# Performance work log

Measured on AMD Instinct MI355X. Metric: run time of the kernel, lower is better.

## Reference

```python
import jax, jax.numpy as jnp
import numpy as np

N = 131072   # total nodes
B = 256      # graphs
NPG = 512    # nodes per graph (N = B*NPG, nodes ordered by graph)
K = 7        # knn neighbors
H = 4        # heads


def setup_inputs() -> dict:
    key = jax.random.key(0)
    ks = jax.random.split(key, 16)
    s = 0.1
    pos = jax.random.normal(ks[0], (N, 3), jnp.float32)
    x = jax.random.normal(ks[1], (N, 10), jnp.float32)
    batch = jnp.repeat(jnp.arange(B, dtype=jnp.int32), NPG)
    # GATv2 layer 1: in=10, out=16, heads=4 -> H*C = 64
    Wl1 = jax.random.normal(ks[2], (10, 64), jnp.float32) * s
    bl1 = jnp.zeros((64,), jnp.float32)
    Wr1 = jax.random.normal(ks[3], (10, 64), jnp.float32) * s
    br1 = jnp.zeros((64,), jnp.float32)
    att1 = jax.random.normal(ks[4], (H, 16), jnp.float32) * s
    bias1 = jnp.zeros((64,), jnp.float32)
    # GATv2 layer 2: in=64, out=32, heads=4 -> H*C = 128
    Wl2 = jax.random.normal(ks[5], (64, 128), jnp.float32) * s
    bl2 = jnp.zeros((128,), jnp.float32)
    Wr2 = jax.random.normal(ks[6], (64, 128), jnp.float32) * s
    br2 = jnp.zeros((128,), jnp.float32)
    att2 = jax.random.normal(ks[7], (H, 32), jnp.float32) * s
    bias2 = jnp.zeros((128,), jnp.float32)
    return dict(pos=pos, x=x, batch=batch,
                Wl1=Wl1, bl1=bl1, Wr1=Wr1, br1=br1, att1=att1, bias1=bias1,
                Wl2=Wl2, bl2=bl2, Wr2=Wr2, br2=br2, att2=att2, bias2=bias2)


def knn_edges(pos):
    # equal-size graphs, nodes ordered by graph -> per-graph brute-force kNN
    p = pos.reshape(B, NPG, -1)                                  # [B,n,3]
    d2 = jnp.sum((p[:, :, None, :] - p[:, None, :, :]) ** 2, -1)  # [B,n,n]
    d2 = d2 + jnp.eye(NPG, dtype=d2.dtype) * 1e10                 # no self-loops
    _, idx = jax.lax.top_k(-d2, K)                                # [B,n,K]
    offs = (jnp.arange(B, dtype=idx.dtype) * NPG)[:, None, None]
    src = (idx + offs).reshape(-1)                                # neighbors -> sources
    dst = jnp.broadcast_to(jnp.arange(N)[:, None], (N, K)).reshape(-1)
    return src, dst


def gatv2(x, src, dst, Wl, bl, Wr, br, att, C):
    xl = (x @ Wl + bl).reshape(N, H, C)   # lin_l -> source features / messages
    xr = (x @ Wr + br).reshape(N, H, C)   # lin_r -> target features
    m = jax.nn.leaky_relu(xl[src] + xr[dst], 0.2)     # [E,H,C]
    alpha = jnp.einsum('ehc,hc->eh', m, att)          # [E,H]
    amax = jax.ops.segment_max(alpha, dst, num_segments=N)
    ea = jnp.exp(alpha - amax[dst])
    denom = jax.ops.segment_sum(ea, dst, num_segments=N)
    a = ea / denom[dst]                               # softmax per destination
    out = jax.ops.segment_sum(a[:, :, None] * xl[src], dst, num_segments=N)
    return out.reshape(N, H * C)


def reference(pos, x, batch, Wl1, bl1, Wr1, br1, att1, bias1,
              Wl2, bl2, Wr2, br2, att2, bias2):
    src, dst = knn_edges(pos)
    h = gatv2(x, src, dst, Wl1, bl1, Wr1, br1, att1, 16) + bias1   # [N,64]
    h = gatv2(h, src, dst, Wl2, bl2, Wr2, br2, att2, 32) + bias2   # [N,128]
    # global mean pool over batch ids
    sums = jax.ops.segment_sum(h, batch, num_segments=B)
    cnts = jax.ops.segment_sum(jnp.ones((N, 1), h.dtype), batch, num_segments=B)
    return sums / cnts                                              # [B,128]
```

## Files before the change

### kernel.cpp

```cpp
#include <hip/hip_runtime.h>
#include <hip/hip_bf16.h>

#define N_NODES 131072
#define B_GRAPHS 256
#define NPG 512
#define KNN 7
#define HEADS 4

using f4 = __attribute__((ext_vector_type(4))) float;
using short8 = __attribute__((ext_vector_type(8))) short;

__device__ __forceinline__ unsigned short f2bf(float f) {
    unsigned u = __builtin_bit_cast(unsigned, f);
    u += 0x7FFFu + ((u >> 16) & 1u);
    return (unsigned short)(u >> 16);
}

__device__ __forceinline__ void s8_to_f(const short8 v, f4* out) {
#pragma unroll
    for (int i = 0; i < 8; ++i) {
        const unsigned u = ((unsigned)(unsigned short)v[i]) << 16;
        out[i >> 2][i & 3] = __builtin_bit_cast(float, u);
    }
}

__device__ __forceinline__ unsigned med3u(unsigned a, unsigned b, unsigned c) {
    unsigned r;
    asm("v_med3_u32 %0, %1, %2, %3" : "=v"(r) : "v"(a), "v"(b), "v"(c));
    return r;
}

#define INS7(B, KEY) { \
    const unsigned _k = (KEY); \
    const unsigned n0 = min(B[0], _k); \
    const unsigned n1 = med3u(B[0], B[1], _k); \
    const unsigned n2 = med3u(B[1], B[2], _k); \
    const unsigned n3 = med3u(B[2], B[3], _k); \
    const unsigned n4 = med3u(B[3], B[4], _k); \
    const unsigned n5 = med3u(B[4], B[5], _k); \
    const unsigned n6 = med3u(B[5], B[6], _k); \
    B[0]=n0; B[1]=n1; B[2]=n2; B[3]=n3; B[4]=n4; B[5]=n5; B[6]=n6; }

__global__ __launch_bounds__(512) void knn_kernel(const float* __restrict__ pos,
                                                  int* __restrict__ knn) {
    __shared__ f4 sp[NPG];
    __shared__ unsigned mk[3][128][7];
    const int tid = threadIdx.x;
    const int g = blockIdx.x >> 2;
    const int qh = blockIdx.x & 3;
    const int ch = tid >> 7;
    const int ql = tid & 127;
    const int q = qh * 128 + ql;

    const float* p = pos + (size_t)g * NPG * 3;
    {
        f4 v; v[0] = p[tid * 3 + 0]; v[1] = p[tid * 3 + 1]; v[2] = p[tid * 3 + 2]; v[3] = 0.f;
        sp[tid] = v;
    }
    __syncthreads();

    const f4 qp = sp[q];
    unsigned b[7];
#pragma unroll
    for (int i = 0; i < 7; ++i) b[i] = 0xFFFFFFFFu;

    const int j0 = ch << 7;
#pragma unroll 8
    for (int j = 0; j < 128; ++j) {
        const int jj = j0 + j;
        const f4 c = sp[jj];
        const float dx = qp[0] - c[0];
        const float dy = qp[1] - c[1];
        const float dz = qp[2] - c[2];
        const float d2 = dx * dx + dy * dy + dz * dz;
        unsigned key = (__builtin_bit_cast(unsigned, d2) & 0xFFFFFE00u) | (unsigned)jj;
        key = (jj == q) ? 0xFFFFFFFFu : key;
        INS7(b, key)
    }

    if (ch != 0) {
        unsigned* m = mk[ch - 1][ql];
#pragma unroll
        for (int i = 0; i < 7; ++i) m[i] = b[i];
    }
    __syncthreads();
    if (ch == 0) {
#pragma unroll
        for (int cc = 0; cc < 3; ++cc) {
            const unsigned* m = mk[cc][ql];
#pragma unroll
            for (int i = 0; i < 7; ++i) INS7(b, m[i])
        }
        const int base = (g * NPG + q) * KNN;
        const int off = g * NPG;
#pragma unroll
        for (int i = 0; i < 7; ++i) knn[base + i] = off + (int)(b[i] & 0x1FFu);
    }
}
#undef INS7

__global__ __launch_bounds__(256) void lin1_kernel(const float* __restrict__ x,
                                                   const float* __restrict__ Wl,
                                                   const float* __restrict__ bl,
                                                   const float* __restrict__ Wr,
                                                   const float* __restrict__ br,
                                                   unsigned short* __restrict__ xl1b,
                                                   float* __restrict__ xr1) {
    const int idx = blockIdx.x * 256 + threadIdx.x;
    const int c4 = idx & 15;
    const size_t node = (size_t)(idx >> 4);
    const float* xrow = x + node * 10;
    f4 al = ((const f4*)bl)[c4];
    f4 ar = ((const f4*)br)[c4];
#pragma unroll
    for (int k = 0; k < 10; ++k) {
        const float xv = xrow[k];
        al += xv * ((const f4*)(Wl + k * 64))[c4];
        ar += xv * ((const f4*)(Wr + k * 64))[c4];
    }
    uint2 pk;
    pk.x = (unsigned)f2bf(al[0]) | ((unsigned)f2bf(al[1]) << 16);
    pk.y = (unsigned)f2bf(al[2]) | ((unsigned)f2bf(al[3]) << 16);
    ((uint2*)xl1b)[node * 16 + c4] = pk;
    ((f4*)(xr1 + node * 64))[c4] = ar;
}

__global__ __launch_bounds__(256) void agg1_kernel(const unsigned short* __restrict__ xl1b,
                                                   const float* __restrict__ xr,
                                                   const int* __restrict__ knn,
                                                   const float* __restrict__ att,
                                                   const float* __restrict__ bias,
                                                   unsigned short* __restrict__ h1b) {
    const int x = blockIdx.x & 7;
    const int i = blockIdx.x >> 3;
    const int graph = x * 32 + (i >> 3);
    const int sub = i & 7;
    const int tid = threadIdx.x;
    const int h = tid & 3;
    const size_t node = (size_t)graph * NPG + sub * 64 + (tid >> 2);

    const int* nb = knn + node * KNN;
    int j[KNN];
#pragma unroll
    for (int k = 0; k < KNN; ++k) j[k] = nb[k];

    f4 xr4[4], at4[4];
    const f4* xrp = (const f4*)(xr + node * 64 + h * 16);
    const f4* atp = (const f4*)(att + h * 16);
#pragma unroll
    for (int i2 = 0; i2 < 4; ++i2) { xr4[i2] = xrp[i2]; at4[i2] = atp[i2]; }

    float alpha[KNN];
#pragma unroll
    for (int k = 0; k < KNN; ++k) {
        const short8* xlp = (const short8*)(xl1b + (size_t)j[k] * 64 + h * 16);
        f4 xlv[4];
        s8_to_f(xlp[0], &xlv[0]);
        s8_to_f(xlp[1], &xlv[2]);
        float s = 0.f;
#pragma unroll
        for (int i2 = 0; i2 < 4; ++i2) {
            const f4 m = xlv[i2] + xr4[i2];
#pragma unroll
            for (int c = 0; c < 4; ++c) {
                float mm = m[c];
                mm = mm > 0.f ? mm : 0.2f * mm;
                s += mm * at4[i2][c];
            }
        }
        alpha[k] = s;
    }
    float amax = alpha[0];
#pragma unroll
    for (int k = 1; k < KNN; ++k) amax = fmaxf(amax, alpha[k]);
    float e[KNN];
    float denom = 0.f;
#pragma unroll
    for (int k = 0; k < KNN; ++k) { e[k] = expf(alpha[k] - amax); denom += e[k]; }
    const float rd = 1.f / denom;

    f4 o4[4];
#pragma unroll
    for (int i2 = 0; i2 < 4; ++i2) o4[i2] = 0.f;
#pragma unroll
    for (int k = 0; k < KNN; ++k) {
        const short8* xlp = (const short8*)(xl1b + (size_t)j[k] * 64 + h * 16);
        f4 xlv[4];
        s8_to_f(xlp[0], &xlv[0]);
        s8_to_f(xlp[1], &xlv[2]);
#pragma unroll
        for (int i2 = 0; i2 < 4; ++i2) o4[i2] += e[k] * xlv[i2];
    }
    const f4* bp = (const f4*)(bias + h * 16);
    short8 r0, r1;
#pragma unroll
    for (int i2 = 0; i2 < 4; ++i2) {
        const f4 v = o4[i2] * rd + bp[i2];
#pragma unroll
        for (int c = 0; c < 4; ++c) {
            const unsigned short bv = f2bf(v[c]);
            const int e4 = i2 * 4 + c;
            if (e4 < 8) r0[e4] = (short)bv; else r1[e4 - 8] = (short)bv;
        }
    }
    short8* hp = (short8*)(h1b + node * 64 + h * 16);
    hp[0] = r0;
    hp[1] = r1;
}

__global__ __launch_bounds__(256) void wprep_kernel(const float* __restrict__ Wl,
                                                    const float* __restrict__ Wr,
                                                    unsigned short* __restrict__ wbf) {
    const int t = blockIdx.x * 256 + threadIdx.x;
    const int k = t >> 8;
    const int n = t & 255;
    const float v = (n < 128) ? Wl[k * 128 + n] : Wr[k * 128 + (n - 128)];
    wbf[((k >> 3) * 256 + n) * 8 + (k & 7)] = f2bf(v);
}

__global__ __launch_bounds__(256) void lin2_kernel(const unsigned short* __restrict__ h1b,
                                                   const unsigned short* __restrict__ wbf,
                                                   const float* __restrict__ bl,
                                                   const float* __restrict__ br,
                                                   unsigned short* __restrict__ xl2b,
                                                   unsigned short* __restrict__ xr2b) {
    const int tid = threadIdx.x;
    const int lane = tid & 63;
    const int w = tid >> 6;
    const size_t node0 = (size_t)blockIdx.x * 16;
    const int lm = lane & 15, lk = lane >> 4;

    const short8* hp = (const short8*)h1b;
    const short8 a0 = hp[(node0 + lm) * 8 + lk];
    const short8 a1 = hp[(node0 + lm) * 8 + lk + 4];

    const short8* wp = (const short8*)wbf;
#pragma unroll
    for (int t = 0; t < 4; ++t) {
        const int col = w * 64 + t * 16 + lm;
        const float bias = (col < 128) ? bl[col] : br[col - 128];
        f4 acc = {bias, bias, bias, bias};
        const short8 b0 = wp[lk * 256 + col];
        const short8 b1 = wp[(lk + 4) * 256 + col];
        acc = __builtin_amdgcn_mfma_f32_16x16x32_bf16(a0, b0, acc, 0, 0, 0);
        acc = __builtin_amdgcn_mfma_f32_16x16x32_bf16(a1, b1, acc, 0, 0, 0);
        unsigned short* dst = (col < 128) ? (xl2b + col) : (xr2b + (col - 128));
#pragma unroll
        for (int r = 0; r < 4; ++r)
            dst[(node0 + lk * 4 + r) * 128] = f2bf(acc[r]);
    }
}

__global__ __launch_bounds__(256) void agg2_pool_kernel(const unsigned short* __restrict__ xl2b,
                                                        const unsigned short* __restrict__ xr2b,
                                                        const int* __restrict__ knn,
                                                        const float* __restrict__ att,
                                                        float* __restrict__ partial) {
    const int x = blockIdx.x & 7;
    const int i = blockIdx.x >> 3;
    const int graph = x * 32 + (i >> 4);
    const int sub = i & 15;
    const int tid = threadIdx.x;
    const int lane = tid & 63;
    const int wv = tid >> 6;
    const int n8 = lane >> 3;
    const int h = (lane >> 1) & 3;
    const int half = lane & 1;
    const size_t node = (size_t)graph * NPG + sub * 32 + wv * 8 + n8;
    const int co = h * 32 + half * 16;

    const int* nb = knn + node * KNN;
    int j[KNN];
#pragma unroll
    for (int k = 0; k < KNN; ++k) j[k] = nb[k];

    f4 xr4[4], at4[4];
    {
        const short8* xrp = (const short8*)(xr2b + node * 128 + co);
        s8_to_f(xrp[0], &xr4[0]);
        s8_to_f(xrp[1], &xr4[2]);
        const f4* atp = (const f4*)(att + co);
#pragma unroll
        for (int i2 = 0; i2 < 4; ++i2) at4[i2] = atp[i2];
    }

    float alpha[KNN];
#pragma unroll
    for (int k = 0; k < KNN; ++k) {
        const short8* xlp = (const short8*)(xl2b + (size_t)j[k] * 128 + co);
        f4 xlv[4];
        s8_to_f(xlp[0], &xlv[0]);
        s8_to_f(xlp[1], &xlv[2]);
        float s = 0.f;
#pragma unroll
        for (int i2 = 0; i2 < 4; ++i2) {
            const f4 m = xlv[i2] + xr4[i2];
#pragma unroll
            for (int c = 0; c < 4; ++c) {
                float mm = m[c];
                mm = mm > 0.f ? mm : 0.2f * mm;
                s += mm * at4[i2][c];
            }
        }
        alpha[k] = s + __shfl_xor(s, 1);
    }
    float amax = alpha[0];
#pragma unroll
    for (int k = 1; k < KNN; ++k) amax = fmaxf(amax, alpha[k]);
    float e[KNN];
    float denom = 0.f;
#pragma unroll
    for (int k = 0; k < KNN; ++k) { e[k] = expf(alpha[k] - amax); denom += e[k]; }
    const float rd = 1.f / denom;

    f4 o4[4];
#pragma unroll
    for (int i2 = 0; i2 < 4; ++i2) o4[i2] = 0.f;
#pragma unroll
    for (int k = 0; k < KNN; ++k) {
        const short8* xlp = (const short8*)(xl2b + (size_t)j[k] * 128 + co);
        f4 xlv[4];
        s8_to_f(xlp[0], &xlv[0]);
        s8_to_f(xlp[1], &xlv[2]);
#pragma unroll
        for (int i2 = 0; i2 < 4; ++i2) o4[i2] += e[k] * xlv[i2];
    }
#pragma unroll
    for (int i2 = 0; i2 < 4; ++i2) o4[i2] *= rd;

#pragma unroll
    for (int m = 8; m <= 32; m <<= 1) {
#pragma unroll
        for (int i2 = 0; i2 < 4; ++i2) {
#pragma unroll
            for (int c = 0; c < 4; ++c) o4[i2][c] += __shfl_xor(o4[i2][c], m);
        }
    }
    if (n8 == 0) {
        f4* pp = (f4*)(partial + ((size_t)(graph * 16 + sub) * 4 + wv) * 128 + co);
#pragma unroll
        for (int i2 = 0; i2 < 4; ++i2) pp[i2] = o4[i2];
    }
}

__global__ __launch_bounds__(128) void pool2_kernel(const float* __restrict__ partial,
                                                    const float* __restrict__ bias,
                                                    float* __restrict__ out) {
    const int g = blockIdx.x;
    const int c = threadIdx.x;
    float s = 0.f;
#pragma unroll
    for (int b = 0; b < 64; ++b) s += partial[(size_t)(g * 64 + b) * 128 + c];
    out[g * 128 + c] = s * (1.f / 512.f) + bias[c];
}

extern "C" void kernel_launch(void* const* d_in, const int* in_sizes, int n_in,
                              void* d_out, int out_size, void* d_ws, size_t ws_size,
                              hipStream_t stream) {
    const float* pos   = (const float*)d_in[0];
    const float* x     = (const float*)d_in[1];
    const float* Wl1   = (const float*)d_in[3];
    const float* bl1   = (const float*)d_in[4];
    const float* Wr1   = (const float*)d_in[5];
    const float* br1   = (const float*)d_in[6];
    const float* att1  = (const float*)d_in[7];
    const float* bias1 = (const float*)d_in[8];
    const float* Wl2   = (const float*)d_in[9];
    const float* bl2   = (const float*)d_in[10];
    const float* Wr2   = (const float*)d_in[11];
    const float* br2   = (const float*)d_in[12];
    const float* att2  = (const float*)d_in[13];
    const float* bias2 = (const float*)d_in[14];
    float* out = (float*)d_out;

    char* ws = (char*)d_ws;
    int*            knn  = (int*)(ws + 0);
    unsigned short* xl1b = (unsigned short*)(ws + 3670016);
    float*          xr1  = (float*)(ws + 20447232);
    unsigned short* h1b  = (unsigned short*)(ws + 54001664);
    unsigned short* wbf  = (unsigned short*)(ws + 70778880);
    unsigned short* xl2b = (unsigned short*)(ws + 88080384);
    unsigned short* xr2b = (unsigned short*)(ws + 121634816);
    float*          partial = (float*)(ws + 54001664);

    knn_kernel<<<B_GRAPHS * 4, 512, 0, stream>>>(pos, knn);
    lin1_kernel<<<(N_NODES * 16) / 256, 256, 0, stream>>>(x, Wl1, bl1, Wr1, br1, xl1b, xr1);
    wprep_kernel<<<64, 256, 0, stream>>>(Wl2, Wr2, wbf);
    agg1_kernel<<<(N_NODES * 4) / 256, 256, 0, stream>>>(xl1b, xr1, knn, att1, bias1, h1b);
    lin2_kernel<<<N_NODES / 16, 256, 0, stream>>>(h1b, wbf, bl2, br2, xl2b, xr2b);
    agg2_pool_kernel<<<N_NODES / 32, 256, 0, stream>>>(xl2b, xr2b, knn, att2, partial);
    pool2_kernel<<<B_GRAPHS, 128, 0, stream>>>(partial, bias2, out);
}
```

Before: 156.6 us.

## Store xr1 in bf16 and spread aggregation over more lanes per node

lin1 now writes the target features xr1 as bf16 rather than fp32, which halves that buffer's write and read traffic. Both aggregation kernels are remapped so each lane handles 8 channels, with 8 lanes per node in agg1 and 16 in agg2. Heads are reduced with shuffle-xor, and each neighbor row is loaded once into registers and reused for the weighted sum. The new mapping gives more parallelism and coalesced 16-byte gathers, at the cost of more shuffles, twice as many partial rows for pool2, and bf16 rounding on xr1.

```diff
diff --git a/kernel.cpp b/kernel.cpp
--- a/kernel.cpp
+++ b/kernel.cpp
@@ -105,7 +105,7 @@
                                                    const float* __restrict__ Wr,
                                                    const float* __restrict__ br,
                                                    unsigned short* __restrict__ xl1b,
-                                                   float* __restrict__ xr1) {
+                                                   unsigned short* __restrict__ xr1b) {
     const int idx = blockIdx.x * 256 + threadIdx.x;
     const int c4 = idx & 15;
     const size_t node = (size_t)(idx >> 4);
@@ -118,48 +118,51 @@
         al += xv * ((const f4*)(Wl + k * 64))[c4];
         ar += xv * ((const f4*)(Wr + k * 64))[c4];
     }
-    uint2 pk;
-    pk.x = (unsigned)f2bf(al[0]) | ((unsigned)f2bf(al[1]) << 16);
-    pk.y = (unsigned)f2bf(al[2]) | ((unsigned)f2bf(al[3]) << 16);
-    ((uint2*)xl1b)[node * 16 + c4] = pk;
-    ((f4*)(xr1 + node * 64))[c4] = ar;
+    uint2 pl, pr;
+    pl.x = (unsigned)f2bf(al[0]) | ((unsigned)f2bf(al[1]) << 16);
+    pl.y = (unsigned)f2bf(al[2]) | ((unsigned)f2bf(al[3]) << 16);
+    pr.x = (unsigned)f2bf(ar[0]) | ((unsigned)f2bf(ar[1]) << 16);
+    pr.y = (unsigned)f2bf(ar[2]) | ((unsigned)f2bf(ar[3]) << 16);
+    ((uint2*)xl1b)[node * 16 + c4] = pl;
+    ((uint2*)xr1b)[node * 16 + c4] = pr;
 }
 
 __global__ __launch_bounds__(256) void agg1_kernel(const unsigned short* __restrict__ xl1b,
-                                                   const float* __restrict__ xr,
+                                                   const unsigned short* __restrict__ xr1b,
                                                    const int* __restrict__ knn,
                                                    const float* __restrict__ att,
                                                    const float* __restrict__ bias,
                                                    unsigned short* __restrict__ h1b) {
     const int x = blockIdx.x & 7;
     const int i = blockIdx.x >> 3;
-    const int graph = x * 32 + (i >> 3);
-    const int sub = i & 7;
+    const int graph = x * 32 + (i >> 4);
+    const int sub = i & 15;
     const int tid = threadIdx.x;
-    const int h = tid & 3;
-    const size_t node = (size_t)graph * NPG + sub * 64 + (tid >> 2);
+    const int lane = tid & 63;
+    const int lc = lane & 7;
+    const size_t node = (size_t)graph * NPG + sub * 32 + (tid >> 3);
+    const int co = lc * 8;
 
     const int* nb = knn + node * KNN;
     int j[KNN];
 #pragma unroll
     for (int k = 0; k < KNN; ++k) j[k] = nb[k];
 
-    f4 xr4[4], at4[4];
-    const f4* xrp = (const f4*)(xr + node * 64 + h * 16);
-    const f4* atp = (const f4*)(att + h * 16);
-#pragma unroll
-    for (int i2 = 0; i2 < 4; ++i2) { xr4[i2] = xrp[i2]; at4[i2] = atp[i2]; }
-
+    f4 xr4[2], at4[2];
+    s8_to_f(*(const short8*)(xr1b + node * 64 + co), xr4);
+    at4[0] = ((const f4*)(att + co))[0];
+    at4[1] = ((const f4*)(att + co))[1];
+
+    short8 xv[KNN];
     float alpha[KNN];
 #pragma unroll
     for (int k = 0; k < KNN; ++k) {
-        const short8* xlp = (const short8*)(xl1b + (size_t)j[k] * 64 + h * 16);
-        f4 xlv[4];
-        s8_to_f(xlp[0], &xlv[0]);
-        s8_to_f(xlp[1], &xlv[2]);
+        xv[k] = *(const short8*)(xl1b + (size_t)j[k] * 64 + co);
+        f4 xlv[2];
+        s8_to_f(xv[k], xlv);
         float s = 0.f;
 #pragma unroll
-        for (int i2 = 0; i2 < 4; ++i2) {
+        for (int i2 = 0; i2 < 2; ++i2) {
             const f4 m = xlv[i2] + xr4[i2];
 #pragma unroll
             for (int c = 0; c < 4; ++c) {
@@ -168,7 +171,7 @@
                 s += mm * at4[i2][c];
             }
         }
-        alpha[k] = s;
+        alpha[k] = s + __shfl_xor(s, 1);
     }
     float amax = alpha[0];
 #pragma unroll
@@ -179,33 +182,23 @@
     for (int k = 0; k < KNN; ++k) { e[k] = expf(alpha[k] - amax); denom += e[k]; }
     const float rd = 1.f / denom;
 
-    f4 o4[4];
-#pragma unroll
-    for (int i2 = 0; i2 < 4; ++i2) o4[i2] = 0.f;
+    f4 o4[2];
+    o4[0] = 0.f; o4[1] = 0.f;
 #pragma unroll
     for (int k = 0; k < KNN; ++k) {
-        const short8* xlp = (const short8*)(xl1b + (size_t)j[k] * 64 + h * 16);
-        f4 xlv[4];
-        s8_to_f(xlp[0], &xlv[0]);
-        s8_to_f(xlp[1], &xlv[2]);
-#pragma unroll
-        for (int i2 = 0; i2 < 4; ++i2) o4[i2] += e[k] * xlv[i2];
-    }
-    const f4* bp = (const f4*)(bias + h * 16);
-    short8 r0, r1;
-#pragma unroll
-    for (int i2 = 0; i2 < 4; ++i2) {
-        const f4 v = o4[i2] * rd + bp[i2];
-#pragma unroll
-        for (int c = 0; c < 4; ++c) {
-            const unsigned short bv = f2bf(v[c]);
-            const int e4 = i2 * 4 + c;
-            if (e4 < 8) r0[e4] = (short)bv; else r1[e4 - 8] = (short)bv;
-        }
-    }
-    short8* hp = (short8*)(h1b + node * 64 + h * 16);
-    hp[0] = r0;
-    hp[1] = r1;
+        f4 xlv[2];
+        s8_to_f(xv[k], xlv);
+        o4[0] += e[k] * xlv[0];
+        o4[1] += e[k] * xlv[1];
+    }
+    short8 r;
+#pragma unroll
+    for (int i2 = 0; i2 < 2; ++i2) {
+        const f4 v = o4[i2] * rd + ((const f4*)(bias + co))[i2];
+#pragma unroll
+        for (int c = 0; c < 4; ++c) r[i2 * 4 + c] = (short)f2bf(v[c]);
+    }
+    *(short8*)(h1b + node * 64 + co) = r;
 }
 
 __global__ __launch_bounds__(256) void wprep_kernel(const float* __restrict__ Wl,
@@ -258,42 +251,36 @@
                                                         float* __restrict__ partial) {
     const int x = blockIdx.x & 7;
     const int i = blockIdx.x >> 3;
-    const int graph = x * 32 + (i >> 4);
-    const int sub = i & 15;
+    const int graph = x * 32 + (i >> 5);
+    const int sub = i & 31;
     const int tid = threadIdx.x;
     const int lane = tid & 63;
     const int wv = tid >> 6;
-    const int n8 = lane >> 3;
-    const int h = (lane >> 1) & 3;
-    const int half = lane & 1;
-    const size_t node = (size_t)graph * NPG + sub * 32 + wv * 8 + n8;
-    const int co = h * 32 + half * 16;
+    const int n4 = lane >> 4;
+    const int lc = lane & 15;
+    const size_t node = (size_t)graph * NPG + sub * 16 + wv * 4 + n4;
+    const int co = lc * 8;
 
     const int* nb = knn + node * KNN;
     int j[KNN];
 #pragma unroll
     for (int k = 0; k < KNN; ++k) j[k] = nb[k];
 
-    f4 xr4[4], at4[4];
-    {
-        const short8* xrp = (const short8*)(xr2b + node * 128 + co);
-        s8_to_f(xrp[0], &xr4[0]);
-        s8_to_f(xrp[1], &xr4[2]);
-        const f4* atp = (const f4*)(att + co);
-#pragma unroll
-        for (int i2 = 0; i2 < 4; ++i2) at4[i2] = atp[i2];
-    }
-
+    f4 xr4[2], at4[2];
+    s8_to_f(*(const short8*)(xr2b + node * 128 + co), xr4);
+    at4[0] = ((const f4*)(att + co))[0];
+    at4[1] = ((const f4*)(att + co))[1];
+
+    short8 xv[KNN];
     float alpha[KNN];
 #pragma unroll
     for (int k = 0; k < KNN; ++k) {
-        const short8* xlp = (const short8*)(xl2b + (size_t)j[k] * 128 + co);
-        f4 xlv[4];
-        s8_to_f(xlp[0], &xlv[0]);
-        s8_to_f(xlp[1], &xlv[2]);
+        xv[k] = *(const short8*)(xl2b + (size_t)j[k] * 128 + co);
+        f4 xlv[2];
+        s8_to_f(xv[k], xlv);
         float s = 0.f;
 #pragma unroll
-        for (int i2 = 0; i2 < 4; ++i2) {
+        for (int i2 = 0; i2 < 2; ++i2) {
             const f4 m = xlv[i2] + xr4[i2];
 #pragma unroll
             for (int c = 0; c < 4; ++c) {
@@ -302,7 +289,8 @@
                 s += mm * at4[i2][c];
             }
         }
-        alpha[k] = s + __shfl_xor(s, 1);
+        s += __shfl_xor(s, 1);
+        alpha[k] = s + __shfl_xor(s, 2);
     }
     float amax = alpha[0];
 #pragma unroll
@@ -313,33 +301,30 @@
     for (int k = 0; k < KNN; ++k) { e[k] = expf(alpha[k] - amax); denom += e[k]; }
     const float rd = 1.f / denom;
 
-    f4 o4[4];
-#pragma unroll
-    for (int i2 = 0; i2 < 4; ++i2) o4[i2] = 0.f;
+    f4 o4[2];
+    o4[0] = 0.f; o4[1] = 0.f;
 #pragma unroll
     for (int k = 0; k < KNN; ++k) {
-        const short8* xlp = (const short8*)(xl2b + (size_t)j[k] * 128 + co);
-        f4 xlv[4];
-        s8_to_f(xlp[0], &xlv[0]);
-        s8_to_f(xlp[1], &xlv[2]);
-#pragma unroll
-        for (int i2 = 0; i2 < 4; ++i2) o4[i2] += e[k] * xlv[i2];
-    }
-#pragma unroll
-    for (int i2 = 0; i2 < 4; ++i2) o4[i2] *= rd;
-
-#pragma unroll
-    for (int m = 8; m <= 32; m <<= 1) {
-#pragma unroll
-        for (int i2 = 0; i2 < 4; ++i2) {
+        f4 xlv[2];
+        s8_to_f(xv[k], xlv);
+        o4[0] += e[k] * xlv[0];
+        o4[1] += e[k] * xlv[1];
+    }
+    o4[0] *= rd;
+    o4[1] *= rd;
+
+#pragma unroll
+    for (int m = 16; m <= 32; m <<= 1) {
+#pragma unroll
+        for (int i2 = 0; i2 < 2; ++i2) {
 #pragma unroll
             for (int c = 0; c < 4; ++c) o4[i2][c] += __shfl_xor(o4[i2][c], m);
         }
     }
-    if (n8 == 0) {
-        f4* pp = (f4*)(partial + ((size_t)(graph * 16 + sub) * 4 + wv) * 128 + co);
-#pragma unroll
-        for (int i2 = 0; i2 < 4; ++i2) pp[i2] = o4[i2];
+    if (n4 == 0) {
+        f4* pp = (f4*)(partial + ((size_t)(graph * 32 + sub) * 4 + wv) * 128 + co);
+        pp[0] = o4[0];
+        pp[1] = o4[1];
     }
 }
 
@@ -350,7 +335,7 @@
     const int c = threadIdx.x;
     float s = 0.f;
 #pragma unroll
-    for (int b = 0; b < 64; ++b) s += partial[(size_t)(g * 64 + b) * 128 + c];
+    for (int b = 0; b < 128; ++b) s += partial[(size_t)(g * 128 + b) * 128 + c];
     out[g * 128 + c] = s * (1.f / 512.f) + bias[c];
 }
 
@@ -376,18 +361,18 @@
     char* ws = (char*)d_ws;
     int*            knn  = (int*)(ws + 0);
     unsigned short* xl1b = (unsigned short*)(ws + 3670016);
-    float*          xr1  = (float*)(ws + 20447232);
-    unsigned short* h1b  = (unsigned short*)(ws + 54001664);
-    unsigned short* wbf  = (unsigned short*)(ws + 70778880);
+    unsigned short* xr1b = (unsigned short*)(ws + 20447232);
+    unsigned short* h1b  = (unsigned short*)(ws + 37224448);
+    unsigned short* wbf  = (unsigned short*)(ws + 54001664);
     unsigned short* xl2b = (unsigned short*)(ws + 88080384);
     unsigned short* xr2b = (unsigned short*)(ws + 121634816);
-    float*          partial = (float*)(ws + 54001664);
+    float*          partial = (float*)(ws + 37224448);
 
     knn_kernel<<<B_GRAPHS * 4, 512, 0, stream>>>(pos, knn);
-    lin1_kernel<<<(N_NODES * 16) / 256, 256, 0, stream>>>(x, Wl1, bl1, Wr1, br1, xl1b, xr1);
+    lin1_kernel<<<(N_NODES * 16) / 256, 256, 0, stream>>>(x, Wl1, bl1, Wr1, br1, xl1b, xr1b);
     wprep_kernel<<<64, 256, 0, stream>>>(Wl2, Wr2, wbf);
-    agg1_kernel<<<(N_NODES * 4) / 256, 256, 0, stream>>>(xl1b, xr1, knn, att1, bias1, h1b);
+    agg1_kernel<<<N_NODES / 32, 256, 0, stream>>>(xl1b, xr1b, knn, att1, bias1, h1b);
     lin2_kernel<<<N_NODES / 16, 256, 0, stream>>>(h1b, wbf, bl2, br2, xl2b, xr2b);
-    agg2_pool_kernel<<<N_NODES / 32, 256, 0, stream>>>(xl2b, xr2b, knn, att2, partial);
+    agg2_pool_kernel<<<N_NODES / 16, 256, 0, stream>>>(xl2b, xr2b, knn, att2, partial);
     pool2_kernel<<<B_GRAPHS, 128, 0, stream>>>(partial, bias2, out);
 }
```

Result: slower. 169.1 us (+8.0%).
